# Performance work log

Hardware: AMD Instinct MI355X
Metric: run time of the kernel (lower is better)

Reference implementation:

```python
import jax, jax.numpy as jnp
import numpy as np

N, M, K, KD = 400000, 300000, 27, 8
CIN, C0, NCLS = 4, 32, 19
EPS = 1e-5


def setup_inputs() -> dict:
    key = jax.random.key(0)
    ks = jax.random.split(key, 20)
    point_fea = jax.random.normal(ks[0], (N, CIN), jnp.float32)
    idx_query = jax.random.randint(ks[1], (N,), 0, M, jnp.int32)
    nbrs = jax.random.randint(ks[2], (M, K), -1, M, jnp.int32)  # -1 = missing neighbor
    idx_dev = jax.random.randint(ks[3], (N, KD), -1, M, jnp.int32)
    w_raw = jax.random.uniform(ks[4], (N, KD), jnp.float32)
    w_dev = w_raw / jnp.sum(w_raw, axis=1, keepdims=True)  # trilinear weights sum to 1
    def w(k, *shape):
        fan = shape[-2] * K if len(shape) == 3 else shape[0]
        return jax.random.normal(k, shape, jnp.float32) / np.sqrt(fan)
    return {
        'point_fea': point_fea, 'idx_query': idx_query, 'nbrs': nbrs,
        'idx_dev': idx_dev, 'w_dev': w_dev,
        'W_s1': w(ks[5], K, CIN, C0), 'W_s2': w(ks[6], K, C0, C0),
        'g_s1': jnp.ones((C0,)), 'b_s1': jnp.zeros((C0,)),
        'g_s2': jnp.ones((C0,)), 'b_s2': jnp.zeros((C0,)),
        'W_r1': w(ks[7], K, C0, C0), 'W_r2': w(ks[8], K, C0, C0),
        'g_r1': jnp.ones((C0,)), 'b_r1': jnp.zeros((C0,)),
        'g_r2': jnp.ones((C0,)), 'b_r2': jnp.zeros((C0,)),
        'W_c': w(ks[9], C0, NCLS), 'b_c': jnp.zeros((NCLS,)),
    }


def sparse_conv(x, W, nbrs):
    # x: [M, Cin], W: [K, Cin, Cout], nbrs: [M, K] (-1 = miss)
    out = jnp.zeros((x.shape[0], W.shape[2]), x.dtype)
    for k in range(W.shape[0]):  # fixed small kernel-offset loop
        idx = nbrs[:, k]
        g = jnp.where((idx >= 0)[:, None], x[jnp.clip(idx, 0)], 0.0)
        out = out + g @ W[k]
    return out


def bn(x, g, b):
    m = jnp.mean(x, axis=0)
    v = jnp.var(x, axis=0)
    return (x - m) * jax.lax.rsqrt(v + EPS) * g + b


def reference(point_fea, idx_query, nbrs, idx_dev, w_dev,
              W_s1, W_s2, g_s1, b_s1, g_s2, b_s2,
              W_r1, W_r2, g_r1, b_r1, g_r2, b_r2, W_c, b_c):
    # spvoxelize: per-voxel mean of point features
    counts = jax.ops.segment_sum(jnp.ones((N,), jnp.float32), idx_query, M)
    vox = jax.ops.segment_sum(point_fea, idx_query, M) / jnp.maximum(counts, 1.0)[:, None]
    # stem: two sparse 3x3x3 convs + BN + ReLU
    h = jax.nn.relu(bn(sparse_conv(vox, W_s1, nbrs), g_s1, b_s1))
    h = jax.nn.relu(bn(sparse_conv(h, W_s2, nbrs), g_s2, b_s2))
    # ResidualBlock (inc == outc, stride 1 -> identity downsample)
    r = jax.nn.relu(bn(sparse_conv(h, W_r1, nbrs), g_r1, b_r1))
    r = bn(sparse_conv(r, W_r2, nbrs), g_r2, b_r2)
    h = jax.nn.relu(r + h)
    # spdevoxelize: masked trilinear 8-neighbor gather back to points
    g = jnp.where((idx_dev >= 0)[:, :, None], h[jnp.clip(idx_dev, 0)], 0.0)  # [N,8,C]
    pts = jnp.einsum('nkc,nk->nc', g, w_dev)
    # classifier
    return pts @ W_c + b_c
```

## Files before the change

kernel.cpp:

```cpp
#include <hip/hip_runtime.h>
#include <hip/hip_fp16.h>

#define NPTS 400000
#define MVOX 300000
#define KK 27
#define KD 8
#define CIN 4
#define C0 32
#define NCLS 19
#define EPS 1e-5f
#define NTILE (MVOX / 16)
#define NPART 512

typedef __attribute__((ext_vector_type(8))) _Float16 half8;
typedef __attribute__((ext_vector_type(4))) float f32x4;

__device__ __forceinline__ uint32_t pack2(float a, float b) {
    __half2 h = __floats2half2_rn(a, b);
    return __builtin_bit_cast(uint32_t, h);
}
__device__ __forceinline__ float2 unpack2(uint32_t u) {
    return __half22float2(__builtin_bit_cast(__half2, u));
}
__device__ __forceinline__ void unpack8(uint4 u, float* f) {
    float2 a = unpack2(u.x), b = unpack2(u.y), c = unpack2(u.z), d = unpack2(u.w);
    f[0] = a.x; f[1] = a.y; f[2] = b.x; f[3] = b.y;
    f[4] = c.x; f[5] = c.y; f[6] = d.x; f[7] = d.y;
}
__device__ __forceinline__ uint4 pack8(const float* f) {
    return make_uint4(pack2(f[0], f[1]), pack2(f[2], f[3]),
                      pack2(f[4], f[5]), pack2(f[6], f[7]));
}

__global__ void vox_accum(const float* __restrict__ pf, const int* __restrict__ iq,
                          float* __restrict__ counts, float* __restrict__ vox) {
    int i = blockIdx.x * blockDim.x + threadIdx.x;
    if (i >= NPTS) return;
    int q = iq[i];
    float4 f = *reinterpret_cast<const float4*>(pf + (size_t)i * CIN);
    atomicAdd(&counts[q], 1.0f);
    atomicAdd(&vox[q * CIN + 0], f.x);
    atomicAdd(&vox[q * CIN + 1], f.y);
    atomicAdd(&vox[q * CIN + 2], f.z);
    atomicAdd(&vox[q * CIN + 3], f.w);
}

__global__ void vox_div_h(const float4* __restrict__ vox, const float* __restrict__ counts,
                          uint2* __restrict__ voxh) {
    int i = blockIdx.x * blockDim.x + threadIdx.x;
    if (i >= MVOX) return;
    float inv = 1.0f / fmaxf(counts[i], 1.0f);
    float4 v = vox[i];
    voxh[i] = make_uint2(pack2(v.x * inv, v.y * inv), pack2(v.z * inv, v.w * inv));
}

__global__ void wprep(const float* __restrict__ W0, const float* __restrict__ W1,
                      const float* __restrict__ W2, uint4* __restrict__ Wf) {
    int t = blockIdx.x * blockDim.x + threadIdx.x;
    if (t >= 3 * KK * 128) return;
    int layer = t / (KK * 128);
    int rem = t % (KK * 128);
    int k = rem / 128;
    int h = (rem >> 6) & 1;
    int lane = rem & 63;
    const float* W = (layer == 0) ? W0 : (layer == 1) ? W1 : W2;
    const float* wk = W + k * (C0 * C0);
    int co = h * 16 + (lane & 15);
    int ci0 = (lane >> 4) * 8;
    float f[8];
#pragma unroll
    for (int j = 0; j < 8; j++) f[j] = wk[(ci0 + j) * C0 + co];
    Wf[t] = pack8(f);
}

__global__ void conv_s1_h(const uint2* __restrict__ x, const int* __restrict__ nbrs,
                          const float* __restrict__ W, uint4* __restrict__ out) {
    int i = blockIdx.x * blockDim.x + threadIdx.x;
    if (i >= MVOX) return;
    float acc[C0];
#pragma unroll
    for (int c = 0; c < C0; c++) acc[c] = 0.f;
    const int* nb = nbrs + (size_t)i * KK;
#pragma unroll
    for (int k = 0; k < KK; k++) {
        int idx = nb[k];
        float m = (idx >= 0) ? 1.f : 0.f;
        uint2 r = x[idx < 0 ? 0 : idx];
        float2 ab = unpack2(r.x), cd = unpack2(r.y);
        float xs[4] = {m * ab.x, m * ab.y, m * cd.x, m * cd.y};
        const float* wk = W + k * (CIN * C0);
#pragma unroll
        for (int j = 0; j < 4; j++) {
#pragma unroll
            for (int co = 0; co < C0; co++) acc[co] += xs[j] * wk[j * C0 + co];
        }
    }
    uint4* o = out + (size_t)i * 4;
#pragma unroll
    for (int p = 0; p < 4; p++) o[p] = pack8(acc + p * 8);
}

__global__ __launch_bounds__(256) void conv32_mfma(const uint4* __restrict__ x,
                                                   const int* __restrict__ nbrs,
                                                   const uint4* __restrict__ Wf,
                                                   const float* __restrict__ ss,
                                                   __half* __restrict__ out) {
    const int lane = threadIdx.x & 63;
    const int wid = threadIdx.x >> 6;
    const int tile = blockIdx.x * 4 + wid;
    if (tile >= NTILE) return;
    const int row = lane & 15;
    const int chunk = lane >> 4;
    float sc[8], sh[8];
#pragma unroll
    for (int j = 0; j < 8; j++) {
        sc[j] = ss[chunk * 8 + j];
        sh[j] = ss[C0 + chunk * 8 + j];
    }
    const int vr = tile * 16 + row;
    const int* nb = nbrs + (size_t)vr * KK;
    f32x4 acc0 = {0.f, 0.f, 0.f, 0.f}, acc1 = {0.f, 0.f, 0.f, 0.f};
#pragma unroll
    for (int k = 0; k < KK; k++) {
        int idx = nb[k];
        float m = (idx >= 0) ? 1.f : 0.f;
        uint4 ar = x[(size_t)(idx < 0 ? 0 : idx) * 4 + chunk];
        float f[8], g[8];
        unpack8(ar, f);
#pragma unroll
        for (int j = 0; j < 8; j++) g[j] = m * fmaxf(f[j] * sc[j] + sh[j], 0.f);
        half8 a = __builtin_bit_cast(half8, pack8(g));
        half8 b0 = __builtin_bit_cast(half8, Wf[k * 128 + lane]);
        half8 b1 = __builtin_bit_cast(half8, Wf[k * 128 + 64 + lane]);
        acc0 = __builtin_amdgcn_mfma_f32_16x16x32_f16(a, b0, acc0, 0, 0, 0);
        acc1 = __builtin_amdgcn_mfma_f32_16x16x32_f16(a, b1, acc1, 0, 0, 0);
    }
    __half* obase = out + (size_t)tile * 16 * C0;
    const int col = lane & 15;
#pragma unroll
    for (int r = 0; r < 4; r++) {
        int orow = chunk * 4 + r;
        obase[orow * C0 + col] = __float2half(acc0[r]);
        obase[orow * C0 + 16 + col] = __float2half(acc1[r]);
    }
}

__global__ __launch_bounds__(256) void bn_partial(const uint4* __restrict__ x,
                                                  float* __restrict__ partials) {
    const int T = MVOX * 4;
    int t0 = blockIdx.x * blockDim.x + threadIdx.x;
    const int stride = NPART * 256;
    float s[8], q[8];
#pragma unroll
    for (int j = 0; j < 8; j++) { s[j] = 0.f; q[j] = 0.f; }
    for (int t = t0; t < T; t += stride) {
        float f[8]; unpack8(x[t], f);
#pragma unroll
        for (int j = 0; j < 8; j++) { s[j] += f[j]; q[j] += f[j] * f[j]; }
    }
#pragma unroll
    for (int off = 32; off >= 4; off >>= 1) {
#pragma unroll
        for (int j = 0; j < 8; j++) {
            s[j] += __shfl_down(s[j], off);
            q[j] += __shfl_down(q[j], off);
        }
    }
    __shared__ float ls[4][64];
    const int w = threadIdx.x >> 6;
    const int lane = threadIdx.x & 63;
    if (lane < 4) {
#pragma unroll
        for (int j = 0; j < 8; j++) {
            ls[w][lane * 8 + j] = s[j];
            ls[w][C0 + lane * 8 + j] = q[j];
        }
    }
    __syncthreads();
    if (threadIdx.x < 64)
        partials[(size_t)blockIdx.x * 64 + threadIdx.x] =
            ls[0][threadIdx.x] + ls[1][threadIdx.x] + ls[2][threadIdx.x] + ls[3][threadIdx.x];
}

__global__ __launch_bounds__(256) void bn_reduce_fin(const float* __restrict__ partials,
                                                     const float* __restrict__ g,
                                                     const float* __restrict__ b,
                                                     float* __restrict__ ss) {
    const int tid = threadIdx.x;
    const int c = tid & 63;
    const int part = tid >> 6;
    float acc = 0.f;
    for (int bk = part; bk < NPART; bk += 4) acc += partials[(size_t)bk * 64 + c];
    __shared__ float ls[4][64];
    ls[part][c] = acc;
    __syncthreads();
    __shared__ float fin[64];
    if (tid < 64) fin[tid] = ls[0][tid] + ls[1][tid] + ls[2][tid] + ls[3][tid];
    __syncthreads();
    if (tid < C0) {
        float mean = fin[tid] * (1.0f / (float)MVOX);
        float var = fin[C0 + tid] * (1.0f / (float)MVOX) - mean * mean;
        float sc = g[tid] * rsqrtf(var + EPS);
        ss[tid] = sc;
        ss[C0 + tid] = b[tid] - mean * sc;
    }
}

__global__ void residual_relu_h(uint4* __restrict__ d, const uint4* __restrict__ braw,
                                const float* __restrict__ ss_r2,
                                const float* __restrict__ ss_s2) {
    int t = blockIdx.x * blockDim.x + threadIdx.x;
    if (t >= MVOX * 4) return;
    int cb = (t & 3) * 8;
    float f[8], h[8];
    unpack8(d[t], f); unpack8(braw[t], h);
#pragma unroll
    for (int j = 0; j < 8; j++) {
        float skip = fmaxf(h[j] * ss_s2[cb + j] + ss_s2[C0 + cb + j], 0.f);
        f[j] = fmaxf(f[j] * ss_r2[cb + j] + ss_r2[C0 + cb + j] + skip, 0.f);
    }
    d[t] = pack8(f);
}

__global__ void devox_classify(const uint4* __restrict__ H, const int4* __restrict__ idxd,
                               const float4* __restrict__ wdev, const float* __restrict__ Wc,
                               const float* __restrict__ bc, float* __restrict__ out) {
    int i = blockIdx.x * blockDim.x + threadIdx.x;
    if (i >= NPTS) return;
    int4 i0 = idxd[2 * i], i1 = idxd[2 * i + 1];
    float4 w0 = wdev[2 * i], w1 = wdev[2 * i + 1];
    int idxs[8] = {i0.x, i0.y, i0.z, i0.w, i1.x, i1.y, i1.z, i1.w};
    float wsv[8] = {w0.x, w0.y, w0.z, w0.w, w1.x, w1.y, w1.z, w1.w};
    float acc[C0];
#pragma unroll
    for (int c = 0; c < C0; c++) acc[c] = 0.f;
#pragma unroll
    for (int k = 0; k < KD; k++) {
        float m = (idxs[k] >= 0) ? wsv[k] : 0.f;
        const uint4* hr = H + (size_t)(idxs[k] < 0 ? 0 : idxs[k]) * 4;
#pragma unroll
        for (int p = 0; p < 4; p++) {
            float f[8]; unpack8(hr[p], f);
#pragma unroll
            for (int j = 0; j < 8; j++) acc[p * 8 + j] += m * f[j];
        }
    }
    float o[NCLS];
#pragma unroll
    for (int c = 0; c < NCLS; c++) o[c] = bc[c];
#pragma unroll
    for (int ci = 0; ci < C0; ci++) {
        float xv = acc[ci];
#pragma unroll
        for (int c = 0; c < NCLS; c++) o[c] += xv * Wc[ci * NCLS + c];
    }
    float* op = out + (size_t)i * NCLS;
#pragma unroll
    for (int c = 0; c < NCLS; c++) op[c] = o[c];
}

extern "C" void kernel_launch(void* const* d_in, const int* in_sizes, int n_in,
                              void* d_out, int out_size, void* d_ws, size_t ws_size,
                              hipStream_t stream) {
    const float* point_fea = (const float*)d_in[0];
    const int*   idx_query = (const int*)d_in[1];
    const int*   nbrs      = (const int*)d_in[2];
    const int*   idx_dev   = (const int*)d_in[3];
    const float* w_dev     = (const float*)d_in[4];
    const float* W_s1      = (const float*)d_in[5];
    const float* W_s2      = (const float*)d_in[6];
    const float* g_s1      = (const float*)d_in[7];
    const float* b_s1      = (const float*)d_in[8];
    const float* g_s2      = (const float*)d_in[9];
    const float* b_s2      = (const float*)d_in[10];
    const float* W_r1      = (const float*)d_in[11];
    const float* W_r2      = (const float*)d_in[12];
    const float* g_r1      = (const float*)d_in[13];
    const float* b_r1      = (const float*)d_in[14];
    const float* g_r2      = (const float*)d_in[15];
    const float* b_r2      = (const float*)d_in[16];
    const float* W_c       = (const float*)d_in[17];
    const float* b_c       = (const float*)d_in[18];
    float* out = (float*)d_out;

    float* ws = (float*)d_ws;
    const size_t M = MVOX;
    float* ss       = ws;
    float* partials = ws + 256;
    float* counts   = partials + NPART * 64;
    float* vox32    = counts + M;
    uint2* voxh     = (uint2*)(vox32 + 4 * M);
    uint4* Wf       = (uint4*)((float*)voxh + 2 * M);
    float* bufs     = (float*)Wf + 3 * KK * 128 * 4;
    uint4* A = (uint4*)bufs;
    uint4* B = A + M * 4;
    uint4* C = B + M * 4;
    uint4* D = C + M * 4;

    hipMemsetAsync(counts, 0, (size_t)(5 * M) * sizeof(float), stream);

    dim3 blk(256);
    dim3 gN((NPTS + 255) / 256);
    dim3 gM((MVOX + 255) / 256);
    dim3 gE((MVOX * 4 + 255) / 256);
    dim3 gT((NTILE + 3) / 4);
    dim3 gW((3 * KK * 128 + 255) / 256);

    vox_accum<<<gN, blk, 0, stream>>>(point_fea, idx_query, counts, vox32);
    vox_div_h<<<gM, blk, 0, stream>>>((const float4*)vox32, counts, voxh);
    wprep<<<gW, blk, 0, stream>>>(W_s2, W_r1, W_r2, Wf);

    conv_s1_h<<<gM, blk, 0, stream>>>(voxh, nbrs, W_s1, A);
    bn_partial<<<NPART, blk, 0, stream>>>(A, partials);
    bn_reduce_fin<<<1, blk, 0, stream>>>(partials, g_s1, b_s1, ss + 0);

    conv32_mfma<<<gT, blk, 0, stream>>>(A, nbrs, Wf + 0 * KK * 128, ss + 0, (__half*)B);
    bn_partial<<<NPART, blk, 0, stream>>>(B, partials);
    bn_reduce_fin<<<1, blk, 0, stream>>>(partials, g_s2, b_s2, ss + 64);

    conv32_mfma<<<gT, blk, 0, stream>>>(B, nbrs, Wf + 1 * KK * 128, ss + 64, (__half*)C);
    bn_partial<<<NPART, blk, 0, stream>>>(C, partials);
    bn_reduce_fin<<<1, blk, 0, stream>>>(partials, g_r1, b_r1, ss + 128);

    conv32_mfma<<<gT, blk, 0, stream>>>(C, nbrs, Wf + 2 * KK * 128, ss + 128, (__half*)D);
    bn_partial<<<NPART, blk, 0, stream>>>(D, partials);
    bn_reduce_fin<<<1, blk, 0, stream>>>(partials, g_r2, b_r2, ss + 192);

    residual_relu_h<<<gE, blk, 0, stream>>>(D, B, ss + 192, ss + 64);

    devox_classify<<<gN, blk, 0, stream>>>(D, (const int4*)idx_dev,
                                           (const float4*)w_dev, W_c, b_c, out);
}
```

Baseline: 798.8 us.

## Fuse BN statistics into conv epilogues and apply classifier before devoxelize gather

Result: slower. 1.004 ms (+25.7%).

```diff
diff --git a/kernel.cpp b/kernel.cpp
--- a/kernel.cpp
+++ b/kernel.cpp
@@ -10,7 +10,8 @@
 #define NCLS 19
 #define EPS 1e-5f
 #define NTILE (MVOX / 16)
-#define NPART 512
+#define GS1 ((MVOX + 255) / 256)
+#define GT ((NTILE + 3) / 4)
 
 typedef __attribute__((ext_vector_type(8))) _Float16 half8;
 typedef __attribute__((ext_vector_type(4))) float f32x4;
@@ -73,108 +74,121 @@
     Wf[t] = pack8(f);
 }
 
-__global__ void conv_s1_h(const uint2* __restrict__ x, const int* __restrict__ nbrs,
-                          const float* __restrict__ W, uint4* __restrict__ out) {
+__global__ __launch_bounds__(256) void conv_s1_h(const uint2* __restrict__ x,
+                                                 const int* __restrict__ nbrs,
+                                                 const float* __restrict__ W,
+                                                 uint4* __restrict__ out,
+                                                 float* __restrict__ partials) {
     int i = blockIdx.x * blockDim.x + threadIdx.x;
-    if (i >= MVOX) return;
+    const bool active = i < MVOX;
     float acc[C0];
 #pragma unroll
     for (int c = 0; c < C0; c++) acc[c] = 0.f;
-    const int* nb = nbrs + (size_t)i * KK;
-#pragma unroll
-    for (int k = 0; k < KK; k++) {
-        int idx = nb[k];
-        float m = (idx >= 0) ? 1.f : 0.f;
-        uint2 r = x[idx < 0 ? 0 : idx];
-        float2 ab = unpack2(r.x), cd = unpack2(r.y);
-        float xs[4] = {m * ab.x, m * ab.y, m * cd.x, m * cd.y};
-        const float* wk = W + k * (CIN * C0);
-#pragma unroll
-        for (int j = 0; j < 4; j++) {
-#pragma unroll
-            for (int co = 0; co < C0; co++) acc[co] += xs[j] * wk[j * C0 + co];
+    if (active) {
+        const int* nb = nbrs + (size_t)i * KK;
+#pragma unroll
+        for (int k = 0; k < KK; k++) {
+            int idx = nb[k];
+            float m = (idx >= 0) ? 1.f : 0.f;
+            uint2 r = x[idx < 0 ? 0 : idx];
+            float2 ab = unpack2(r.x), cd = unpack2(r.y);
+            float xs[4] = {m * ab.x, m * ab.y, m * cd.x, m * cd.y};
+            const float* wk = W + k * (CIN * C0);
+#pragma unroll
+            for (int j = 0; j < 4; j++) {
+#pragma unroll
+                for (int co = 0; co < C0; co++) acc[co] += xs[j] * wk[j * C0 + co];
+            }
         }
-    }
-    uint4* o = out + (size_t)i * 4;
-#pragma unroll
-    for (int p = 0; p < 4; p++) o[p] = pack8(acc + p * 8);
+        uint4* o = out + (size_t)i * 4;
+#pragma unroll
+        for (int p = 0; p < 4; p++) o[p] = pack8(acc + p * 8);
+    }
+    float q[C0];
+#pragma unroll
+    for (int c = 0; c < C0; c++) q[c] = acc[c] * acc[c];
+#pragma unroll
+    for (int off = 32; off >= 1; off >>= 1) {
+#pragma unroll
+        for (int c = 0; c < C0; c++) {
+            acc[c] += __shfl_down(acc[c], off);
+            q[c] += __shfl_down(q[c], off);
+        }
+    }
+    __shared__ float ls[4][64];
+    const int wid = threadIdx.x >> 6, lane = threadIdx.x & 63;
+    if (lane == 0) {
+#pragma unroll
+        for (int c = 0; c < C0; c++) { ls[wid][c] = acc[c]; ls[wid][C0 + c] = q[c]; }
+    }
+    __syncthreads();
+    if (threadIdx.x < 64)
+        partials[(size_t)blockIdx.x * 64 + threadIdx.x] =
+            ls[0][threadIdx.x] + ls[1][threadIdx.x] + ls[2][threadIdx.x] + ls[3][threadIdx.x];
 }
 
 __global__ __launch_bounds__(256) void conv32_mfma(const uint4* __restrict__ x,
                                                    const int* __restrict__ nbrs,
                                                    const uint4* __restrict__ Wf,
                                                    const float* __restrict__ ss,
-                                                   __half* __restrict__ out) {
+                                                   __half* __restrict__ out,
+                                                   float* __restrict__ partials) {
     const int lane = threadIdx.x & 63;
     const int wid = threadIdx.x >> 6;
     const int tile = blockIdx.x * 4 + wid;
-    if (tile >= NTILE) return;
+    const bool active = tile < NTILE;
     const int row = lane & 15;
     const int chunk = lane >> 4;
+    const int col = lane & 15;
     float sc[8], sh[8];
 #pragma unroll
     for (int j = 0; j < 8; j++) {
         sc[j] = ss[chunk * 8 + j];
         sh[j] = ss[C0 + chunk * 8 + j];
     }
-    const int vr = tile * 16 + row;
-    const int* nb = nbrs + (size_t)vr * KK;
     f32x4 acc0 = {0.f, 0.f, 0.f, 0.f}, acc1 = {0.f, 0.f, 0.f, 0.f};
-#pragma unroll
-    for (int k = 0; k < KK; k++) {
-        int idx = nb[k];
-        float m = (idx >= 0) ? 1.f : 0.f;
-        uint4 ar = x[(size_t)(idx < 0 ? 0 : idx) * 4 + chunk];
-        float f[8], g[8];
-        unpack8(ar, f);
-#pragma unroll
-        for (int j = 0; j < 8; j++) g[j] = m * fmaxf(f[j] * sc[j] + sh[j], 0.f);
-        half8 a = __builtin_bit_cast(half8, pack8(g));
-        half8 b0 = __builtin_bit_cast(half8, Wf[k * 128 + lane]);
-        half8 b1 = __builtin_bit_cast(half8, Wf[k * 128 + 64 + lane]);
-        acc0 = __builtin_amdgcn_mfma_f32_16x16x32_f16(a, b0, acc0, 0, 0, 0);
-        acc1 = __builtin_amdgcn_mfma_f32_16x16x32_f16(a, b1, acc1, 0, 0, 0);
-    }
-    __half* obase = out + (size_t)tile * 16 * C0;
-    const int col = lane & 15;
+    if (active) {
+        const int vr = tile * 16 + row;
+        const int* nb = nbrs + (size_t)vr * KK;
+#pragma unroll
+        for (int k = 0; k < KK; k++) {
+            int idx = nb[k];
+            float m = (idx >= 0) ? 1.f : 0.f;
+            uint4 ar = x[(size_t)(idx < 0 ? 0 : idx) * 4 + chunk];
+            float f[8], g[8];
+            unpack8(ar, f);
+#pragma unroll
+            for (int j = 0; j < 8; j++) g[j] = m * fmaxf(f[j] * sc[j] + sh[j], 0.f);
+            half8 a = __builtin_bit_cast(half8, pack8(g));
+            half8 b0 = __builtin_bit_cast(half8, Wf[k * 128 + lane]);
+            half8 b1 = __builtin_bit_cast(half8, Wf[k * 128 + 64 + lane]);
+            acc0 = __builtin_amdgcn_mfma_f32_16x16x32_f16(a, b0, acc0, 0, 0, 0);
+            acc1 = __builtin_amdgcn_mfma_f32_16x16x32_f16(a, b1, acc1, 0, 0, 0);
+        }
+        __half* obase = out + (size_t)tile * 16 * C0;
+#pragma unroll
+        for (int r = 0; r < 4; r++) {
+            int orow = chunk * 4 + r;
+            obase[orow * C0 + col] = __float2half(acc0[r]);
+            obase[orow * C0 + 16 + col] = __float2half(acc1[r]);
+        }
+    }
+    float s0 = 0.f, q0 = 0.f, s1 = 0.f, q1 = 0.f;
 #pragma unroll
     for (int r = 0; r < 4; r++) {
-        int orow = chunk * 4 + r;
-        obase[orow * C0 + col] = __float2half(acc0[r]);
-        obase[orow * C0 + 16 + col] = __float2half(acc1[r]);
-    }
-}
-
-__global__ __launch_bounds__(256) void bn_partial(const uint4* __restrict__ x,
-                                                  float* __restrict__ partials) {
-    const int T = MVOX * 4;
-    int t0 = blockIdx.x * blockDim.x + threadIdx.x;
-    const int stride = NPART * 256;
-    float s[8], q[8];
-#pragma unroll
-    for (int j = 0; j < 8; j++) { s[j] = 0.f; q[j] = 0.f; }
-    for (int t = t0; t < T; t += stride) {
-        float f[8]; unpack8(x[t], f);
-#pragma unroll
-        for (int j = 0; j < 8; j++) { s[j] += f[j]; q[j] += f[j] * f[j]; }
-    }
-#pragma unroll
-    for (int off = 32; off >= 4; off >>= 1) {
-#pragma unroll
-        for (int j = 0; j < 8; j++) {
-            s[j] += __shfl_down(s[j], off);
-            q[j] += __shfl_down(q[j], off);
-        }
-    }
+        s0 += acc0[r]; q0 += acc0[r] * acc0[r];
+        s1 += acc1[r]; q1 += acc1[r] * acc1[r];
+    }
+    s0 += __shfl_xor(s0, 16); q0 += __shfl_xor(q0, 16);
+    s1 += __shfl_xor(s1, 16); q1 += __shfl_xor(q1, 16);
+    s0 += __shfl_xor(s0, 32); q0 += __shfl_xor(q0, 32);
+    s1 += __shfl_xor(s1, 32); q1 += __shfl_xor(q1, 32);
     __shared__ float ls[4][64];
-    const int w = threadIdx.x >> 6;
-    const int lane = threadIdx.x & 63;
-    if (lane < 4) {
-#pragma unroll
-        for (int j = 0; j < 8; j++) {
-            ls[w][lane * 8 + j] = s[j];
-            ls[w][C0 + lane * 8 + j] = q[j];
-        }
+    if (lane < 16) {
+        ls[wid][col] = s0;
+        ls[wid][16 + col] = s1;
+        ls[wid][32 + col] = q0;
+        ls[wid][48 + col] = q1;
     }
     __syncthreads();
     if (threadIdx.x < 64)
@@ -182,81 +196,104 @@
             ls[0][threadIdx.x] + ls[1][threadIdx.x] + ls[2][threadIdx.x] + ls[3][threadIdx.x];
 }
 
-__global__ __launch_bounds__(256) void bn_reduce_fin(const float* __restrict__ partials,
-                                                     const float* __restrict__ g,
-                                                     const float* __restrict__ b,
-                                                     float* __restrict__ ss) {
+__global__ __launch_bounds__(1024) void bn_reduce_fin(const float* __restrict__ partials,
+                                                      int nblocks,
+                                                      const float* __restrict__ g,
+                                                      const float* __restrict__ b,
+                                                      float* __restrict__ ss) {
     const int tid = threadIdx.x;
     const int c = tid & 63;
     const int part = tid >> 6;
     float acc = 0.f;
-    for (int bk = part; bk < NPART; bk += 4) acc += partials[(size_t)bk * 64 + c];
-    __shared__ float ls[4][64];
+    for (int bk = part; bk < nblocks; bk += 16) acc += partials[(size_t)bk * 64 + c];
+    __shared__ float ls[16][64];
     ls[part][c] = acc;
     __syncthreads();
     __shared__ float fin[64];
-    if (tid < 64) fin[tid] = ls[0][tid] + ls[1][tid] + ls[2][tid] + ls[3][tid];
+    if (tid < 64) {
+        float t = 0.f;
+#pragma unroll
+        for (int p = 0; p < 16; p++) t += ls[p][tid];
+        fin[tid] = t;
+    }
     __syncthreads();
     if (tid < C0) {
         float mean = fin[tid] * (1.0f / (float)MVOX);
         float var = fin[C0 + tid] * (1.0f / (float)MVOX) - mean * mean;
-        float sc = g[tid] * rsqrtf(var + EPS);
-        ss[tid] = sc;
-        ss[C0 + tid] = b[tid] - mean * sc;
-    }
-}
-
-__global__ void residual_relu_h(uint4* __restrict__ d, const uint4* __restrict__ braw,
-                                const float* __restrict__ ss_r2,
-                                const float* __restrict__ ss_s2) {
-    int t = blockIdx.x * blockDim.x + threadIdx.x;
-    if (t >= MVOX * 4) return;
-    int cb = (t & 3) * 8;
-    float f[8], h[8];
-    unpack8(d[t], f); unpack8(braw[t], h);
-#pragma unroll
-    for (int j = 0; j < 8; j++) {
-        float skip = fmaxf(h[j] * ss_s2[cb + j] + ss_s2[C0 + cb + j], 0.f);
-        f[j] = fmaxf(f[j] * ss_r2[cb + j] + ss_r2[C0 + cb + j] + skip, 0.f);
-    }
-    d[t] = pack8(f);
-}
-
-__global__ void devox_classify(const uint4* __restrict__ H, const int4* __restrict__ idxd,
-                               const float4* __restrict__ wdev, const float* __restrict__ Wc,
-                               const float* __restrict__ bc, float* __restrict__ out) {
+        float scv = g[tid] * rsqrtf(var + EPS);
+        ss[tid] = scv;
+        ss[C0 + tid] = b[tid] - mean * scv;
+    }
+}
+
+__global__ __launch_bounds__(256) void classify_pre(const uint4* __restrict__ D,
+                                                    const uint4* __restrict__ B,
+                                                    const float* __restrict__ ss_r2,
+                                                    const float* __restrict__ ss_s2,
+                                                    const float* __restrict__ Wc,
+                                                    uint4* __restrict__ HC) {
+    int v = blockIdx.x * blockDim.x + threadIdx.x;
+    if (v >= MVOX) return;
+    float f[C0], h[C0];
+#pragma unroll
+    for (int p = 0; p < 4; p++) {
+        float tf[8], th[8];
+        unpack8(D[(size_t)v * 4 + p], tf);
+        unpack8(B[(size_t)v * 4 + p], th);
+#pragma unroll
+        for (int j = 0; j < 8; j++) { f[p * 8 + j] = tf[j]; h[p * 8 + j] = th[j]; }
+    }
+    float hh[C0];
+#pragma unroll
+    for (int j = 0; j < C0; j++) {
+        float skip = fmaxf(h[j] * ss_s2[j] + ss_s2[C0 + j], 0.f);
+        hh[j] = fmaxf(f[j] * ss_r2[j] + ss_r2[C0 + j] + skip, 0.f);
+    }
+    float o[20];
+#pragma unroll
+    for (int c = 0; c < 20; c++) o[c] = 0.f;
+#pragma unroll
+    for (int ci = 0; ci < C0; ci++) {
+        float xv = hh[ci];
+#pragma unroll
+        for (int c = 0; c < NCLS; c++) o[c] += xv * Wc[ci * NCLS + c];
+    }
+    uint4* dst = HC + (size_t)v * 4;
+    dst[0] = pack8(o);
+    dst[1] = pack8(o + 8);
+    *reinterpret_cast<uint2*>(dst + 2) = make_uint2(pack2(o[16], o[17]), pack2(o[18], 0.f));
+}
+
+__global__ __launch_bounds__(256) void devox_out(const uint4* __restrict__ HC,
+                                                 const int4* __restrict__ idxd,
+                                                 const float4* __restrict__ wdev,
+                                                 const float* __restrict__ bc,
+                                                 float* __restrict__ out) {
     int i = blockIdx.x * blockDim.x + threadIdx.x;
     if (i >= NPTS) return;
     int4 i0 = idxd[2 * i], i1 = idxd[2 * i + 1];
     float4 w0 = wdev[2 * i], w1 = wdev[2 * i + 1];
     int idxs[8] = {i0.x, i0.y, i0.z, i0.w, i1.x, i1.y, i1.z, i1.w};
     float wsv[8] = {w0.x, w0.y, w0.z, w0.w, w1.x, w1.y, w1.z, w1.w};
-    float acc[C0];
-#pragma unroll
-    for (int c = 0; c < C0; c++) acc[c] = 0.f;
+    float acc[20];
+#pragma unroll
+    for (int c = 0; c < 20; c++) acc[c] = 0.f;
 #pragma unroll
     for (int k = 0; k < KD; k++) {
         float m = (idxs[k] >= 0) ? wsv[k] : 0.f;
-        const uint4* hr = H + (size_t)(idxs[k] < 0 ? 0 : idxs[k]) * 4;
-#pragma unroll
-        for (int p = 0; p < 4; p++) {
-            float f[8]; unpack8(hr[p], f);
-#pragma unroll
-            for (int j = 0; j < 8; j++) acc[p * 8 + j] += m * f[j];
-        }
-    }
-    float o[NCLS];
-#pragma unroll
-    for (int c = 0; c < NCLS; c++) o[c] = bc[c];
-#pragma unroll
-    for (int ci = 0; ci < C0; ci++) {
-        float xv = acc[ci];
-#pragma unroll
-        for (int c = 0; c < NCLS; c++) o[c] += xv * Wc[ci * NCLS + c];
+        const uint4* hr = HC + (size_t)(idxs[k] < 0 ? 0 : idxs[k]) * 4;
+        uint4 a = hr[0], b2 = hr[1];
+        uint2 cp = *reinterpret_cast<const uint2*>(hr + 2);
+        float fa[8], fb[8];
+        unpack8(a, fa); unpack8(b2, fb);
+#pragma unroll
+        for (int j = 0; j < 8; j++) { acc[j] += m * fa[j]; acc[8 + j] += m * fb[j]; }
+        float2 t0 = unpack2(cp.x), t1 = unpack2(cp.y);
+        acc[16] += m * t0.x; acc[17] += m * t0.y; acc[18] += m * t1.x;
     }
     float* op = out + (size_t)i * NCLS;
 #pragma unroll
-    for (int c = 0; c < NCLS; c++) op[c] = o[c];
+    for (int c = 0; c < NCLS; c++) op[c] = acc[c] + bc[c];
 }
 
 extern "C" void kernel_launch(void* const* d_in, const int* in_sizes, int n_in,
@@ -287,11 +324,11 @@
     const size_t M = MVOX;
     float* ss       = ws;
     float* partials = ws + 256;
-    float* counts   = partials + NPART * 64;
+    float* counts   = partials + (size_t)GT * 64;
     float* vox32    = counts + M;
     uint2* voxh     = (uint2*)(vox32 + 4 * M);
     uint4* Wf       = (uint4*)((float*)voxh + 2 * M);
-    float* bufs     = (float*)Wf + 3 * KK * 128 * 4;
+    float* bufs     = (float*)Wf + (size_t)3 * KK * 128 * 4;
     uint4* A = (uint4*)bufs;
     uint4* B = A + M * 4;
     uint4* C = B + M * 4;
@@ -301,33 +338,28 @@
 
     dim3 blk(256);
     dim3 gN((NPTS + 255) / 256);
-    dim3 gM((MVOX + 255) / 256);
-    dim3 gE((MVOX * 4 + 255) / 256);
-    dim3 gT((NTILE + 3) / 4);
+    dim3 gM(GS1);
+    dim3 gT(GT);
     dim3 gW((3 * KK * 128 + 255) / 256);
 
     vox_accum<<<gN, blk, 0, stream>>>(point_fea, idx_query, counts, vox32);
     vox_div_h<<<gM, blk, 0, stream>>>((const float4*)vox32, counts, voxh);
     wprep<<<gW, blk, 0, stream>>>(W_s2, W_r1, W_r2, Wf);
 
-    conv_s1_h<<<gM, blk, 0, stream>>>(voxh, nbrs, W_s1, A);
-    bn_partial<<<NPART, blk, 0, stream>>>(A, partials);
-    bn_reduce_fin<<<1, blk, 0, stream>>>(partials, g_s1, b_s1, ss + 0);
-
-    conv32_mfma<<<gT, blk, 0, stream>>>(A, nbrs, Wf + 0 * KK * 128, ss + 0, (__half*)B);
-    bn_partial<<<NPART, blk, 0, stream>>>(B, partials);
-    bn_reduce_fin<<<1, blk, 0, stream>>>(partials, g_s2, b_s2, ss + 64);
-
-    conv32_mfma<<<gT, blk, 0, stream>>>(B, nbrs, Wf + 1 * KK * 128, ss + 64, (__half*)C);
-    bn_partial<<<NPART, blk, 0, stream>>>(C, partials);
-    bn_reduce_fin<<<1, blk, 0, stream>>>(partials, g_r1, b_r1, ss + 128);
-
-    conv32_mfma<<<gT, blk, 0, stream>>>(C, nbrs, Wf + 2 * KK * 128, ss + 128, (__half*)D);
-    bn_partial<<<NPART, blk, 0, stream>>>(D, partials);
-    bn_reduce_fin<<<1, blk, 0, stream>>>(partials, g_r2, b_r2, ss + 192);
-
-    residual_relu_h<<<gE, blk, 0, stream>>>(D, B, ss + 192, ss + 64);
-
-    devox_classify<<<gN, blk, 0, stream>>>(D, (const int4*)idx_dev,
-                                           (const float4*)w_dev, W_c, b_c, out);
-}
+    conv_s1_h<<<gM, blk, 0, stream>>>(voxh, nbrs, W_s1, A, partials);
+    bn_reduce_fin<<<1, 1024, 0, stream>>>(partials, GS1, g_s1, b_s1, ss + 0);
+
+    conv32_mfma<<<gT, blk, 0, stream>>>(A, nbrs, Wf + 0 * KK * 128, ss + 0, (__half*)B, partials);
+    bn_reduce_fin<<<1, 1024, 0, stream>>>(partials, GT, g_s2, b_s2, ss + 64);
+
+    conv32_mfma<<<gT, blk, 0, stream>>>(B, nbrs, Wf + 1 * KK * 128, ss + 64, (__half*)C, partials);
+    bn_reduce_fin<<<1, 1024, 0, stream>>>(partials, GT, g_r1, b_r1, ss + 128);
+
+    conv32_mfma<<<gT, blk, 0, stream>>>(C, nbrs, Wf + 2 * KK * 128, ss + 128, (__half*)D, partials);
+    bn_reduce_fin<<<1, 1024, 0, stream>>>(partials, GT, g_r2, b_r2, ss + 192);
+
+    classify_pre<<<gM, blk, 0, stream>>>(D, B, ss + 192, ss + 64, W_c, A);
+
+    devox_out<<<gN, blk, 0, stream>>>(A, (const int4*)idx_dev,
+                                      (const float4*)w_dev, b_c, out);
+}
```
